# Performance work log

Hardware: AMD Instinct MI355X
Metric: run time of the kernel (lower is better)

The kernel has to match this reference:

```python
import jax, jax.numpy as jnp
import numpy as np
import math

# ---------- real Clebsch-Gordan coupling tables (computed once, tiny) ----------
def _cg(j1, m1, j2, m2, j3, m3):
    if m1 + m2 != m3 or j3 < abs(j1 - j2) or j3 > j1 + j2:
        return 0.0
    f = math.factorial
    pre = ((2 * j3 + 1) * f(j3 + j1 - j2) * f(j3 - j1 + j2) * f(j1 + j2 - j3) / f(j1 + j2 + j3 + 1)) ** 0.5
    pre *= (f(j3 + m3) * f(j3 - m3) * f(j1 - m1) * f(j1 + m1) * f(j2 - m2) * f(j2 + m2)) ** 0.5
    s = 0.0
    for k in range(0, j1 + j2 - j3 + 1):
        d = (k, j1 + j2 - j3 - k, j1 - m1 - k, j2 + m2 - k, j3 - j2 + m1 + k, j3 - j1 - m2 + k)
        if min(d) < 0:
            continue
        den = 1
        for t in d:
            den *= f(t)
        s += (-1) ** k / den
    return pre * s

def _Q(l):  # complex->real spherical-harmonic change of basis
    Q = np.zeros((2 * l + 1, 2 * l + 1), dtype=complex)
    Q[l, l] = 1.0
    s = 2 ** -0.5
    for m in range(1, l + 1):
        Q[l + m, l + m] = (-1) ** m * s
        Q[l + m, l - m] = s
        Q[l - m, l + m] = -1j * (-1) ** m * s
        Q[l - m, l - m] = 1j * s
    return Q

def _K(l1, l2, l3):  # real coupling tensor [2l3+1, 2l1+1, 2l2+1]
    C = np.zeros((2 * l3 + 1, 2 * l1 + 1, 2 * l2 + 1), dtype=complex)
    for M3 in range(-l3, l3 + 1):
        for M1 in range(-l1, l1 + 1):
            for M2 in range(-l2, l2 + 1):
                C[M3 + l3, M1 + l1, M2 + l2] = _cg(l1, M1, l2, M2, l3, M3)
    K = np.einsum('cC,aA,bB,CAB->cab', _Q(l3).conj(), _Q(l1), _Q(l2), C)
    K = K.imag if np.abs(K.imag).max() > np.abs(K.real).max() else K.real
    return np.asarray(K, dtype=np.float32)

# the 9 'uvu' instructions (in_l, edge_l, out_l) with multiplicities (weight_numel=144)
_PATHS = [(0, 0, 0), (0, 2, 2), (1, 0, 1), (1, 2, 1), (1, 2, 2), (2, 0, 2), (2, 2, 0), (2, 2, 1), (2, 2, 2)]
_KT = [jnp.asarray(_K(*p)) for p in _PATHS]
_MULS = [32, 32, 16, 16, 16, 8, 8, 8, 8]
_SPLITS = np.cumsum(_MULS)[:-1].tolist()
NEI = 8
EPS = 1e-5

def _sh(u):  # component-normalized real SH of unit vectors, l=0..2 (m order -l..l, l=1 -> y,z,x)
    x, y, z = u[:, 0], u[:, 1], u[:, 2]
    sh0 = jnp.ones_like(x)[:, None]
    sh1 = np.float32(3 ** 0.5) * jnp.stack([y, z, x], -1)
    s15 = np.float32(15 ** 0.5)
    s5 = np.float32(5 ** 0.5)
    sh2 = jnp.stack([s15 * x * y, s15 * y * z, 0.5 * s5 * (3 * z * z - 1.0), s15 * x * z, 0.5 * s15 * (x * x - y * y)], -1)
    return sh0, sh1, sh2

def _path(xs, sh, wp, Kt):  # xs [E,u,2l1+1], sh [E,2l2+1], Kt [2l3+1,2l1+1,2l2+1] -> [E,u,2l3+1]
    return jnp.einsum('eui,ej,oij->euo', xs, sh, Kt) * wp[None, :, None]

def _layer(x0, x1, x2, pos, src, dst, w, W0, W1, W2, bw0, bb0, bw1, bw2, N):
    ev = pos[dst] - pos[src]
    u = ev / (jnp.linalg.norm(ev, axis=1, keepdims=True) + 1e-12)
    sh0, sh1, sh2 = _sh(u)
    s0 = x0[src][:, :, None]  # [E,32,1]
    s1 = x1[src]              # [E,16,3]
    s2 = x2[src]              # [E,8,5]
    ws = jnp.split(w, _SPLITS)
    p1 = _path(s0, sh0, ws[0], _KT[0])
    p2 = _path(s0, sh2, ws[1], _KT[1])
    p3 = _path(s1, sh0, ws[2], _KT[2])
    p4 = _path(s1, sh2, ws[3], _KT[3])
    p5 = _path(s1, sh2, ws[4], _KT[4])
    p6 = _path(s2, sh0, ws[5], _KT[5])
    p7 = _path(s2, sh2, ws[6], _KT[6])
    p8 = _path(s2, sh2, ws[7], _KT[7])
    p9 = _path(s2, sh2, ws[8], _KT[8])
    m0 = jnp.concatenate([p1, p7], 1)          # [E,40,1]
    m1 = jnp.concatenate([p3, p4, p8], 1)      # [E,40,3]
    m2 = jnp.concatenate([p2, p5, p6, p9], 1)  # [E,64,5]
    a0 = jax.ops.segment_sum(m0, dst, num_segments=N)
    a1 = jax.ops.segment_sum(m1, dst, num_segments=N)
    a2 = jax.ops.segment_sum(m2, dst, num_segments=N)
    y0 = (a0[:, :, 0] @ W0) * np.float32(1.0 / 40 ** 0.5)
    y1 = jnp.einsum('num,uv->nvm', a1, W1) * np.float32(1.0 / 40 ** 0.5)
    y2 = jnp.einsum('num,uv->nvm', a2, W2) * np.float32(1.0 / 64 ** 0.5)
    # equivariant batchnorm (training stats): scalars -> standard BN, l>0 -> norm BN
    f = y0 - y0.mean(0)
    y0 = f / jnp.sqrt((f * f).mean(0) + EPS) * bw0 + bb0
    y1 = y1 / jnp.sqrt((y1 * y1).mean(axis=(0, 2)) + EPS)[None, :, None] * bw1[None, :, None]
    y2 = y2 / jnp.sqrt((y2 * y2).mean(axis=(0, 2)) + EPS)[None, :, None] * bw2[None, :, None]
    return y0, y1, y2

def _forward(positions, W_emb, tp_w, lin_W0, lin_W1, lin_W2, bn_w0, bn_b0, bn_w1, bn_w2, Wf1, Wf2, bf2, Wf3, bf3):
    B, P, _ = positions.shape
    N = B * P
    pos = positions.reshape(N, 3)
    # kNN graph from dense cdist + topk (indices are not differentiated)
    pg = jax.lax.stop_gradient(pos)
    sq = jnp.sum(pg * pg, 1)
    d2 = sq[:, None] + sq[None, :] - 2.0 * (pg @ pg.T)
    _, idx = jax.lax.top_k(-d2, NEI + 1)  # smallest distances; col 0 is self
    src = jnp.repeat(jnp.arange(N), NEI)
    dst = idx[:, 1:].reshape(-1)
    x0 = jnp.ones((N, 1), jnp.float32) @ W_emb  # embedding: only 0e->0e path exists
    x1 = jnp.zeros((N, 16, 3), jnp.float32)
    x2 = jnp.zeros((N, 8, 5), jnp.float32)
    for l in range(3):
        y0, y1, y2 = _layer(x0, x1, x2, pos, src, dst, tp_w[l], lin_W0[l], lin_W1[l], lin_W2[l],
                            bn_w0[l], bn_b0[l], bn_w1[l], bn_w2[l], N)
        x0 = jax.nn.relu(y0) + x0
        x1 = jax.nn.relu(y1) + x1
        x2 = jax.nn.relu(y2) + x2
    h = jax.nn.relu((x0 @ Wf1) * np.float32(1.0 / 32 ** 0.5))  # scalar part -> 32x0e
    h = jax.nn.relu(h @ Wf2 + bf2)
    out = (h @ Wf3 + bf3).reshape(B, P, 2)
    return out

def setup_inputs() -> dict:
    key = jax.random.key(0)
    ks = jax.random.split(key, 16)
    B, P = 4, 2048
    return {
        'positions': jax.random.normal(ks[0], (B, P, 3), jnp.float32) * 3.0,
        'W_emb': jax.random.normal(ks[1], (1, 32), jnp.float32),
        'tp_w': jax.random.normal(ks[2], (3, 144), jnp.float32),
        'lin_W0': jax.random.normal(ks[3], (3, 40, 32), jnp.float32),
        'lin_W1': jax.random.normal(ks[4], (3, 40, 16), jnp.float32),
        'lin_W2': jax.random.normal(ks[5], (3, 64, 8), jnp.float32),
        'bn_w0': 1.0 + 0.05 * jax.random.normal(ks[6], (3, 32), jnp.float32),
        'bn_b0': jnp.zeros((3, 32), jnp.float32),
        'bn_w1': 1.0 + 0.05 * jax.random.normal(ks[7], (3, 16), jnp.float32),
        'bn_w2': 1.0 + 0.05 * jax.random.normal(ks[8], (3, 8), jnp.float32),
        'Wf1': jax.random.normal(ks[9], (32, 32), jnp.float32),
        'Wf2': jax.random.normal(ks[10], (32, 16), jnp.float32) * 0.2,
        'bf2': jax.random.normal(ks[11], (16,), jnp.float32) * 0.1,
        'Wf3': jax.random.normal(ks[12], (16, 2), jnp.float32) * 0.2,
        'bf3': jax.random.normal(ks[13], (2,), jnp.float32) * 0.1,
    }

def reference(positions, W_emb, tp_w, lin_W0, lin_W1, lin_W2, bn_w0, bn_b0, bn_w1, bn_w2, Wf1, Wf2, bf2, Wf3, bf3):
    return _forward(positions, W_emb, tp_w, lin_W0, lin_W1, lin_W2, bn_w0, bn_b0, bn_w1, bn_w2, Wf1, Wf2, bf2, Wf3, bf3)
```

## Files before the change

### kernel.cpp

```cpp
#include <hip/hip_runtime.h>
#include <math.h>

#define NN 8192
#define REV_CAP 48
#define KNN_CAP 384
#define PF 12

static const size_t OFF_K     = 0;
static const size_t OFF_CNT   = 512;
static const size_t OFF_REV   = 8704;
static const size_t OFF_STATS = 401920;
static const size_t OFF_XF    = 406528;
static const size_t OFF_YF    = 1389568;
static const size_t WS_FLOATS = 2372608;

static double h_dfact(int n){ double r=1.0; for(int i=2;i<=n;++i) r*=(double)i; return r; }

static double h_dcg(int j1,int m1,int j2,int m2,int j3,int m3){
  if (m1+m2!=m3) return 0.0;
  if (j3 < abs(j1-j2) || j3 > j1+j2) return 0.0;
  double pre = sqrt((double)(2*j3+1)*h_dfact(j3+j1-j2)*h_dfact(j3-j1+j2)*h_dfact(j1+j2-j3)/h_dfact(j1+j2+j3+1));
  pre *= sqrt(h_dfact(j3+m3)*h_dfact(j3-m3)*h_dfact(j1-m1)*h_dfact(j1+m1)*h_dfact(j2-m2)*h_dfact(j2+m2));
  double s=0.0;
  for(int k=0;k<=j1+j2-j3;++k){
    int d1=j1+j2-j3-k, d2=j1-m1-k, d3=j2+m2-k, d4=j3-j2+m1+k, d5=j3-j1-m2+k;
    if(d1<0||d2<0||d3<0||d4<0||d5<0) continue;
    double den = h_dfact(k)*h_dfact(d1)*h_dfact(d2)*h_dfact(d3)*h_dfact(d4)*h_dfact(d5);
    s += ((k&1)? -1.0: 1.0)/den;
  }
  return pre*s;
}

static int h_qrow(int l,int r,int* col,double* re,double* im){
  const double s = 0.70710678118654752440;
  if (r==l){ col[0]=l; re[0]=1.0; im[0]=0.0; return 1; }
  if (r>l){ int m=r-l;
    col[0]=l+m; re[0]=((m&1)?-s:s); im[0]=0.0;
    col[1]=l-m; re[1]=s;            im[1]=0.0;
  } else { int m=l-r;
    col[0]=l+m; re[0]=0.0; im[0]=((m&1)? s : -s);
    col[1]=l-m; re[1]=0.0; im[1]=s;
  }
  return 2;
}

static float g_Khost[405];
static bool  g_Kinit = false;

static void h_computeK(){
  const int sizes[9]={1,25,9,45,75,25,25,75,125};
  const int l1s[9]={0,0,1,1,1,2,2,2,2};
  const int l2s[9]={0,2,0,2,2,0,2,2,2};
  const int l3s[9]={0,2,1,1,2,2,0,1,2};
  for(int tid=0; tid<405; ++tid){
    int p=0, rem=tid;
    for(p=0;p<9;++p){ if(rem < sizes[p]) break; rem -= sizes[p]; }
    const int l1=l1s[p], l2=l2s[p], l3=l3s[p];
    const int n1=2*l1+1, n2=2*l2+1;
    const int c = rem/(n1*n2); const int r2 = rem%(n1*n2); const int a=r2/n2; const int b=r2%n2;

    int c3[2],c1[2],c2[2]; double re3[2],im3[2],re1[2],im1[2],re2[2],im2[2];
    const int nc3 = h_qrow(l3,c,c3,re3,im3);
    const int nc1 = h_qrow(l1,a,c1,re1,im1);
    const int nc2 = h_qrow(l2,b,c2,re2,im2);

    double accRe=0, accIm=0;
    for(int i3=0;i3<nc3;++i3){
      const double q3re=re3[i3], q3im=-im3[i3];
      for(int i1=0;i1<nc1;++i1){
        const double pre_re = q3re*re1[i1] - q3im*im1[i1];
        const double pre_im = q3re*im1[i1] + q3im*re1[i1];
        for(int i2=0;i2<nc2;++i2){
          const double cgv = h_dcg(l1, c1[i1]-l1, l2, c2[i2]-l2, l3, c3[i3]-l3);
          if (cgv==0.0) continue;
          accRe += (pre_re*re2[i2] - pre_im*im2[i2])*cgv;
          accIm += (pre_re*im2[i2] + pre_im*re2[i2])*cgv;
        }
      }
    }
    const bool useImag = ((l1+l2+l3)&1)!=0;
    g_Khost[tid] = (float)(useImag? accIm : accRe);
  }
}

__global__ __launch_bounds__(256) void k_setup(const float* __restrict__ pos,
        const float* __restrict__ W_emb,
        float* __restrict__ xf,
        float* __restrict__ xs, float* __restrict__ ys, float* __restrict__ zs,
        float* __restrict__ qs,
        int* __restrict__ cnt, float* __restrict__ stats){
  int idx = blockIdx.x*256 + threadIdx.x;
  if (idx < 983040) { const int c = idx%120; xf[idx] = (c<32)? W_emb[c] : 0.f; return; }
  idx -= 983040;
  if (idx < 8192) {
    const float x=pos[3*idx], y=pos[3*idx+1], z=pos[3*idx+2];
    xs[idx]=x; ys[idx]=y; zs[idx]=z; qs[idx]=0.5f*(x*x+y*y+z*z);
    return;
  }
  idx -= 8192;
  if (idx < 8192) { cnt[idx]=0; return; }
  idx -= 8192;
  if (idx < 3072) stats[idx]=0.f;
}

__device__ __forceinline__ unsigned fkey(float f){
  const unsigned b = __float_as_uint(f);
  return (b & 0x80000000u) ? ~b : (b | 0x80000000u);
}

#define RSELECT_PUSH(KMAX) do{ \
  unsigned P = 0u; int need = 9; \
  _Pragma("unroll 1") \
  for(int bit=31; bit>=0; --bit){ \
    const unsigned pref = P >> bit; \
    int c0 = 0; \
    _Pragma("unroll") \
    for(int k=0;k<KMAX;++k) c0 += __popcll(__ballot((ku[k]>>bit)==pref)); \
    if (need > c0){ need -= c0; P |= (1u<<bit); } \
  } \
  int c_eq = 0; \
  _Pragma("unroll") \
  for(int k=0;k<KMAX;++k) c_eq += __popcll(__ballot(ku[k]==P)); \
  bool tsel[KMAX]; \
  _Pragma("unroll") \
  for(int k=0;k<KMAX;++k) tsel[k] = (ku[k]==P); \
  if (c_eq > need){ \
    _Pragma("unroll") \
    for(int k=0;k<KMAX;++k) tsel[k]=false; \
    for(int r=0;r<need;++r){ \
      int mid = 0x7fffffff; \
      _Pragma("unroll") \
      for(int k=0;k<KMAX;++k) if (ku[k]==P && !tsel[k] && il[k]<mid) mid = il[k]; \
      _Pragma("unroll") \
      for(int s=32;s>0;s>>=1){ const int om = __shfl_xor(mid,s,64); mid = (om<mid)? om : mid; } \
      _Pragma("unroll") \
      for(int k=0;k<KMAX;++k) if (ku[k]==P && il[k]==mid) tsel[k]=true; \
    } \
  } \
  _Pragma("unroll") \
  for(int k=0;k<KMAX;++k){ \
    const bool take = (ku[k] < P) || tsel[k]; \
    const int ix = il[k]; \
    if (take && ix != node){ \
      int cpos = atomicAdd(&cnt[ix],1); \
      if (cpos < REV_CAP) rev[ix*REV_CAP + cpos] = node; \
    } \
  } \
}while(0)

__global__ __launch_bounds__(256, 8) void k_knn8(const float* __restrict__ xs,
                                              const float* __restrict__ ys,
                                              const float* __restrict__ zs,
                                              const float* __restrict__ qs,
                                              int* __restrict__ cnt, int* __restrict__ rev){
  const int lane = threadIdx.x & 63;
  const int w    = threadIdx.x >> 6;
  const int node = blockIdx.x*4 + w;
  __shared__ float sdist[4][KNN_CAP];
  __shared__ int   sidx[4][KNN_CAP];
  __shared__ int   scount[4];
  if (threadIdx.x < 4) scount[threadIdx.x]=0;
  __syncthreads();

  const float px = xs[node], py = ys[node], pz = zs[node];

  float m1 = INFINITY, m2 = INFINITY;
  for(int c=0;c<4;++c){
    const int base = (c*64 + lane)*4;
    const float4 fx = *(const float4*)(xs + base);
    const float4 fy = *(const float4*)(ys + base);
    const float4 fz = *(const float4*)(zs + base);
    const float4 fq = *(const float4*)(qs + base);
    float ss[4];
    ss[0] = fmaf(-px,fx.x, fmaf(-py,fy.x, fmaf(-pz,fz.x, fq.x)));
    ss[1] = fmaf(-px,fx.y, fmaf(-py,fy.y, fmaf(-pz,fz.y, fq.y)));
    ss[2] = fmaf(-px,fx.z, fmaf(-py,fy.z, fmaf(-pz,fz.z, fq.z)));
    ss[3] = fmaf(-px,fx.w, fmaf(-py,fy.w, fmaf(-pz,fz.w, fq.w)));
    #pragma unroll
    for(int q=0;q<4;++q){
      const float hi = fmaxf(m1, ss[q]);
      m1 = fminf(m1, ss[q]);
      m2 = fminf(m2, hi);
    }
  }
  {
    const unsigned kk1 = fkey(m1), kk2 = fkey(m2);
    unsigned P = 0u; int need = 9;
    #pragma unroll 1
    for(int bit=31; bit>=0; --bit){
      const unsigned pref = P >> bit;
      const int c0 = __popcll(__ballot((kk1>>bit)==pref)) + __popcll(__ballot((kk2>>bit)==pref));
      if (need > c0){ need -= c0; P |= (1u<<bit); }
    }
    m1 = __uint_as_float((P & 0x80000000u) ? (P & 0x7fffffffu) : ~P);
  }
  const float T = m1;

  {
    const int b0 = lane*4;
    float4 nfx = *(const float4*)(xs + b0);
    float4 nfy = *(const float4*)(ys + b0);
    float4 nfz = *(const float4*)(zs + b0);
    float4 nfq = *(const float4*)(qs + b0);
    for(int c=0;c<32;++c){
      const float4 fx=nfx, fy=nfy, fz=nfz, fq=nfq;
      const int cbase = (c*64 + lane)*4;
      if (c<31){
        const int nb2 = ((c+1)*64 + lane)*4;
        nfx = *(const float4*)(xs + nb2);
        nfy = *(const float4*)(ys + nb2);
        nfz = *(const float4*)(zs + nb2);
        nfq = *(const float4*)(qs + nb2);
      }
      float ss[4];
      ss[0] = fmaf(-px,fx.x, fmaf(-py,fy.x, fmaf(-pz,fz.x, fq.x)));
      ss[1] = fmaf(-px,fx.y, fmaf(-py,fy.y, fmaf(-pz,fz.y, fq.y)));
      ss[2] = fmaf(-px,fx.z, fmaf(-py,fy.z, fmaf(-pz,fz.z, fq.z)));
      ss[3] = fmaf(-px,fx.w, fmaf(-py,fy.w, fmaf(-pz,fz.w, fq.w)));
      #pragma unroll
      for(int q=0;q<4;++q){
        if (ss[q] <= T){
          int pos = atomicAdd(&scount[w],1);
          if (pos < KNN_CAP){ sdist[w][pos]=ss[q]; sidx[w][pos]=cbase+q; }
        }
      }
    }
  }
  __syncthreads();

  int m = scount[w]; if (m > KNN_CAP) m = KNN_CAP;
  unsigned ku[KNN_CAP/64]; int il[KNN_CAP/64];
  #pragma unroll
  for(int k=0;k<KNN_CAP/64;++k){
    const int j = lane + 64*k;
    if (j < m){ ku[k]=fkey(sdist[w][j]); il[k]=sidx[w][j]; }
    else      { ku[k]=0xffffffffu;       il[k]=0x7fffffff; }
  }
  if (m <= 128) RSELECT_PUSH(2);
  else          RSELECT_PUSH(6);
}

__global__ __launch_bounds__(256) void k_msg(
  const float* __restrict__ pos,
  const int* __restrict__ cnt, const int* __restrict__ rev,
  const float* __restrict__ Kbuf,
  const float* __restrict__ xf,
  const float* __restrict__ tpw,
  const float* __restrict__ W0, const float* __restrict__ W1, const float* __restrict__ W2,
  float* __restrict__ pA, float* __restrict__ pB,
  float* __restrict__ yf)
{
  const int t = threadIdx.x;
  const int w = t >> 6;
  const int lane = t & 63;
  const int n = blockIdx.x*4 + w;

  __shared__ float KL[405];
  __shared__ float TW[144];
  __shared__ float momPS[4][720];
  __shared__ float aS[4][480];
  __shared__ int   eIdx[4][REV_CAP];
  __shared__ float eSh[4][5][REV_CAP];
  __shared__ float bA[32], bB[96];
  for(int q=t;q<405;q+=256) KL[q]=Kbuf[q];
  for(int q=t;q<144;q+=256) TW[q]=tpw[q];
  if (t<96){ bB[t]=0.f; if(t<32) bA[t]=0.f; }

  const int deg0 = cnt[n];
  const int deg = (deg0<REV_CAP)? deg0 : REV_CAP;
  const float pnx=pos[3*n], pny=pos[3*n+1], pnz=pos[3*n+2];
  const float s15 = 3.8729833462f, s5c = 2.2360679775f;
  if (lane < deg){
    const int i = rev[n*REV_CAP+lane];
    eIdx[w][lane] = i;
    const float ex = pnx - pos[3*i], ey = pny - pos[3*i+1], ez = pnz - pos[3*i+2];
    const float rn = sqrtf(ex*ex+ey*ey+ez*ez) + 1e-12f;
    const float ux=ex/rn, uy=ey/rn, uz=ez/rn;
    eSh[w][0][lane]=s15*ux*uy;
    eSh[w][1][lane]=s15*uy*uz;
    eSh[w][2][lane]=0.5f*s5c*(3.f*uz*uz-1.f);
    eSh[w][3][lane]=s15*ux*uz;
    eSh[w][4][lane]=0.5f*s15*(ux*ux-uy*uy);
  }
  __syncthreads();

  const int c0 = lane*2;
  float mp0=0.f, mp1=0.f;
  float ms0[5], ms1[5];
  #pragma unroll
  for(int j=0;j<5;++j){ ms0[j]=0.f; ms1[j]=0.f; }

  int idxr[PF];
  #pragma unroll
  for(int k=0;k<PF;++k) idxr[k] = (k<deg)? eIdx[w][k] : 0;
  float2 fr[PF];
  if (lane<60){
    #pragma unroll
    for(int k=0;k<PF;++k) fr[k] = *(const float2*)(xf + (size_t)idxr[k]*120 + c0);
  }
  #pragma unroll
  for(int k=0;k<PF;++k){
    if (k<deg){
      const float sh0=eSh[w][0][k], sh1=eSh[w][1][k], sh2=eSh[w][2][k];
      const float sh3=eSh[w][3][k], sh4=eSh[w][4][k];
      if (lane<60){
        const float2 f = fr[k];
        mp0 += f.x; mp1 += f.y;
        ms0[0]+=f.x*sh0; ms0[1]+=f.x*sh1; ms0[2]+=f.x*sh2; ms0[3]+=f.x*sh3; ms0[4]+=f.x*sh4;
        ms1[0]+=f.y*sh0; ms1[1]+=f.y*sh1; ms1[2]+=f.y*sh2; ms1[3]+=f.y*sh3; ms1[4]+=f.y*sh4;
      }
    }
  }
  for(int e=PF;e<deg;++e){
    const int i = eIdx[w][e];
    const float sh0=eSh[w][0][e], sh1=eSh[w][1][e], sh2=eSh[w][2][e];
    const float sh3=eSh[w][3][e], sh4=eSh[w][4][e];
    if (lane<60){
      const float2 f = *(const float2*)(xf + (size_t)i*120 + c0);
      mp0 += f.x; mp1 += f.y;
      ms0[0]+=f.x*sh0; ms0[1]+=f.x*sh1; ms0[2]+=f.x*sh2; ms0[3]+=f.x*sh3; ms0[4]+=f.x*sh4;
      ms1[0]+=f.y*sh0; ms1[1]+=f.y*sh1; ms1[2]+=f.y*sh2; ms1[3]+=f.y*sh3; ms1[4]+=f.y*sh4;
    }
  }
  if (lane<60){
    momPS[w][c0]=mp0; momPS[w][c0+1]=mp1;
    #pragma unroll
    for(int j=0;j<5;++j){ momPS[w][120+c0*5+j]=ms0[j]; momPS[w][120+(c0+1)*5+j]=ms1[j]; }
  }
  __syncthreads();

  #pragma unroll 1
  for(int e=lane; e<480; e+=64){
    int a, b, L, dst; float rw;
    if (e<32){        const int u=e;                            a=0;        b=u;                  L=1;  rw=TW[u];     dst=u; }
    else if (e<192){  const int i=e-32,  u=i/5, o=i%5;          a=1+o*5;    b=120+u*5;            L=5;  rw=TW[32+u];  dst=160+u*5+o; }
    else if (e<240){  const int i=e-192, u=i/3, o=i%3;          a=26+o*3;   b=32+u*3;             L=3;  rw=TW[64+u];  dst=40+u*3+o; }
    else if (e<288){  const int i=e-240, u=i/3, o=i%3;          a=35+o*15;  b=120+(32+u*3)*5;     L=15; rw=TW[80+u];  dst=40+(16+u)*3+o; }
    else if (e<368){  const int i=e-288, u=i/5, o=i%5;          a=80+o*15;  b=120+(32+u*3)*5;     L=15; rw=TW[96+u];  dst=160+(32+u)*5+o; }
    else if (e<408){  const int i=e-368, u=i/5, o=i%5;          a=155+o*5;  b=80+u*5;             L=5;  rw=TW[112+u]; dst=160+(48+u)*5+o; }
    else if (e<416){  const int u=e-408;                        a=180;      b=120+(80+u*5)*5;     L=25; rw=TW[120+u]; dst=32+u; }
    else if (e<440){  const int i=e-416, u=i/3, o=i%3;          a=205+o*25; b=120+(80+u*5)*5;     L=25; rw=TW[128+u]; dst=40+(32+u)*3+o; }
    else {            const int i=e-440, u=i/5, o=i%5;          a=280+o*25; b=120+(80+u*5)*5;     L=25; rw=TW[136+u]; dst=160+(56+u)*5+o; }
    float g=0.f;
    #pragma unroll 1
    for(int k=0;k<L;++k) g += KL[a+k]*momPS[w][b+k];
    aS[w][dst] = rw*g;
  }
  __syncthreads();

  const float inv40 = 0.15811388300841896660f;
  for(int q=lane;q<120;q+=64){
    float out; int chan;
    if (q<32){
      float g=0.f;
      for(int uu=0;uu<40;++uu) g += aS[w][uu]*W0[uu*32+q];
      out = g*inv40; chan = q;
    } else if (q<80){
      const int e=q-32, v=e/3, m=e%3;
      float g=0.f;
      for(int uu=0;uu<40;++uu) g += aS[w][40+uu*3+m]*W1[uu*16+v];
      out = g*inv40; chan = 32+v;
    } else {
      const int e=q-80, tt=e/5, m=e%5;
      float g=0.f;
      for(int uu=0;uu<64;++uu) g += aS[w][160+uu*5+m]*W2[uu*8+tt];
      out = g*0.125f; chan = 48+tt;
    }
    yf[(size_t)n*120+q] = out;
    atomicAdd(&bB[chan], out*out);
    if (q<32) atomicAdd(&bA[q], out);
  }
  __syncthreads();
  if (t<96){
    const int slot = blockIdx.x & 7;
    atomicAdd(&pB[slot*96 + t], bB[t]);
    if (t<32) atomicAdd(&pA[slot*32 + t], bA[t]);
  }
}

__global__ __launch_bounds__(256) void k_norm(const float* __restrict__ yf,
                       const float* __restrict__ pA, const float* __restrict__ pB,
                       const float* __restrict__ bw0,const float* __restrict__ bb0,
                       const float* __restrict__ bw1,const float* __restrict__ bw2,
                       float* __restrict__ xf){
  __shared__ float sc[96], sf[32];
  const int t = threadIdx.x;
  if (t<96){
    float sB=0.f;
    #pragma unroll
    for(int k=0;k<8;++k) sB += pB[k*96+t];
    float scale;
    if (t<32){
      float sA=0.f;
      #pragma unroll
      for(int k=0;k<8;++k) sA += pA[k*32+t];
      const float mean = sA*(1.f/8192.f);
      const float var  = sB*(1.f/8192.f) - mean*mean;
      const float inv  = 1.f/sqrtf(var+1e-5f);
      scale = bw0[t]*inv;
      sf[t] = bb0[t] - mean*scale;
    } else if (t<48){
      scale = bw1[t-32]/sqrtf(sB*(1.f/(8192.f*3.f))+1e-5f);
    } else {
      scale = bw2[t-48]/sqrtf(sB*(1.f/(8192.f*5.f))+1e-5f);
    }
    sc[t]=scale;
  }
  __syncthreads();
  const int idx = blockIdx.x*256 + t;
  if (idx >= NN*120) return;
  const int c = idx%120;
  const int chan = (c<32)? c : ((c<80)? 32+(c-32)/3 : 48+(c-80)/5);
  const float v = yf[idx]*sc[chan] + ((c<32)? sf[c] : 0.f);
  xf[idx] += fmaxf(v,0.f);
}

__global__ __launch_bounds__(256) void k_normmlp(const float* __restrict__ yf,
                                             const float* __restrict__ xf,
                                             const float* __restrict__ pA, const float* __restrict__ pB,
                                             const float* __restrict__ bw0,const float* __restrict__ bb0,
                                             const float* __restrict__ Wf1,const float* __restrict__ Wf2,
                                             const float* __restrict__ bf2,const float* __restrict__ Wf3,
                                             const float* __restrict__ bf3, float* __restrict__ out){
  __shared__ float w1[1024], w2[512], w3[32], b2[16], b3[2], sc0[32], sf0[32];
  const int t=threadIdx.x;
  for(int q=t;q<1024;q+=256) w1[q]=Wf1[q];
  for(int q=t;q<512;q+=256)  w2[q]=Wf2[q];
  if(t<32) w3[t]=Wf3[t];
  if(t<16) b2[t]=bf2[t];
  if(t<2)  b3[t]=bf3[t];
  if(t<32){
    float sA=0.f, sB=0.f;
    #pragma unroll
    for(int k=0;k<8;++k){ sA += pA[k*32+t]; sB += pB[k*96+t]; }
    const float mean = sA*(1.f/8192.f);
    const float var  = sB*(1.f/8192.f) - mean*mean;
    const float inv  = 1.f/sqrtf(var+1e-5f);
    sc0[t] = bw0[t]*inv;
    sf0[t] = bb0[t] - mean*sc0[t];
  }
  __syncthreads();
  const int n = blockIdx.x*256+t;
  if(n>=NN) return;
  float xv[32];
  #pragma unroll
  for(int k=0;k<32;++k){
    const float v = yf[(size_t)n*120+k]*sc0[k] + sf0[k];
    xv[k] = xf[(size_t)n*120+k] + fmaxf(v,0.f);
  }
  const float inv32 = 0.17677669529663688110f;
  float h1[32];
  #pragma unroll 4
  for(int c=0;c<32;++c){ float g=0.f;
    #pragma unroll
    for(int k=0;k<32;++k) g+=xv[k]*w1[k*32+c];
    h1[c]=fmaxf(g*inv32,0.f); }
  float h2[16];
  #pragma unroll 4
  for(int c=0;c<16;++c){ float g=b2[c];
    #pragma unroll
    for(int k=0;k<32;++k) g+=h1[k]*w2[k*16+c];
    h2[c]=fmaxf(g,0.f); }
  #pragma unroll
  for(int m=0;m<2;++m){ float g=b3[m];
    #pragma unroll
    for(int k=0;k<16;++k) g+=h2[k]*w3[k*2+m];
    out[n*2+m]=g; }
}

extern "C" void kernel_launch(void* const* d_in, const int* in_sizes, int n_in,
                              void* d_out, int out_size, void* d_ws, size_t ws_size,
                              hipStream_t stream) {
  const float* positions = (const float*)d_in[0];
  const float* W_emb  = (const float*)d_in[1];
  const float* tp_w   = (const float*)d_in[2];
  const float* lin_W0 = (const float*)d_in[3];
  const float* lin_W1 = (const float*)d_in[4];
  const float* lin_W2 = (const float*)d_in[5];
  const float* bn_w0  = (const float*)d_in[6];
  const float* bn_b0  = (const float*)d_in[7];
  const float* bn_w1  = (const float*)d_in[8];
  const float* bn_w2  = (const float*)d_in[9];
  const float* Wf1 = (const float*)d_in[10];
  const float* Wf2 = (const float*)d_in[11];
  const float* bf2 = (const float*)d_in[12];
  const float* Wf3 = (const float*)d_in[13];
  const float* bf3 = (const float*)d_in[14];

  if (ws_size < WS_FLOATS*sizeof(float)) return;

  float* ws    = (float*)d_ws;
  float* Kbuf  = ws + OFF_K;
  int*   cnt   = (int*)(ws + OFF_CNT);
  int*   rev   = (int*)(ws + OFF_REV);
  float* stats = ws + OFF_STATS;
  float* xf = ws + OFF_XF;
  float* yf = ws + OFF_YF;

  float* xs = yf;
  float* ysA = yf + NN;
  float* zs = yf + 2*NN;
  float* qs = yf + 3*NN;

  if (!g_Kinit){ h_computeK(); g_Kinit = true; }
  hipMemcpyAsync(Kbuf, g_Khost, 405*sizeof(float), hipMemcpyHostToDevice, stream);

  k_setup<<<3916,256,0,stream>>>(positions, W_emb, xf, xs, ysA, zs, qs, cnt, stats);
  k_knn8<<<NN/4,256,0,stream>>>(xs, ysA, zs, qs, cnt, rev);

  for(int l=0;l<3;++l){
    float* pA = stats + l*1024;
    float* pB = pA + 256;
    k_msg<<<NN/4,256,0,stream>>>(positions, cnt, rev, Kbuf, xf,
                              tp_w + l*144, lin_W0 + l*40*32, lin_W1 + l*40*16, lin_W2 + l*64*8,
                              pA, pB, yf);
    if (l<2){
      k_norm<<<(NN*120+255)/256,256,0,stream>>>(yf, pA, pB,
                              bn_w0 + l*32, bn_b0 + l*32, bn_w1 + l*16, bn_w2 + l*8,
                              xf);
    }
  }
  k_normmlp<<<NN/256,256,0,stream>>>(yf, xf, stats + 2*1024, stats + 2*1024 + 256,
                              bn_w0 + 64, bn_b0 + 64,
                              Wf1, Wf2, bf2, Wf3, bf3, (float*)d_out);
}
```

Measured before the change: 277.3 us.

## Process two query nodes per wavefront in kNN and parallelize final MLP per node

The kNN kernel now has each wavefront handle two query nodes, so every candidate position load serves two distance computations. This halves global/L2 traffic per node at the cost of more registers and twice the shared candidate buffers per block. The final norm+MLP kernel switches from one thread per node with large register arrays to one wavefront per node, with lanes computing output channels through shared memory. That raises parallelism for the 8192-node tail kernel but adds block-wide syncs and leaves most lanes idle.

```diff
diff --git a/kernel.cpp b/kernel.cpp
--- a/kernel.cpp
+++ b/kernel.cpp
@@ -106,6 +106,18 @@
 __device__ __forceinline__ unsigned fkey(float f){
   const unsigned b = __float_as_uint(f);
   return (b & 0x80000000u) ? ~b : (b | 0x80000000u);
+}
+
+__device__ __forceinline__ float rsel9_T(float m1, float m2){
+  const unsigned kk1 = fkey(m1), kk2 = fkey(m2);
+  unsigned P = 0u; int need = 9;
+  #pragma unroll 1
+  for(int bit=31; bit>=0; --bit){
+    const unsigned pref = P >> bit;
+    const int c0 = __popcll(__ballot((kk1>>bit)==pref)) + __popcll(__ballot((kk2>>bit)==pref));
+    if (need > c0){ need -= c0; P |= (1u<<bit); }
+  }
+  return __uint_as_float((P & 0x80000000u) ? (P & 0x7fffffffu) : ~P);
 }
 
 #define RSELECT_PUSH(KMAX) do{ \
@@ -155,46 +167,39 @@
                                               int* __restrict__ cnt, int* __restrict__ rev){
   const int lane = threadIdx.x & 63;
   const int w    = threadIdx.x >> 6;
-  const int node = blockIdx.x*4 + w;
-  __shared__ float sdist[4][KNN_CAP];
-  __shared__ int   sidx[4][KNN_CAP];
-  __shared__ int   scount[4];
-  if (threadIdx.x < 4) scount[threadIdx.x]=0;
-  __syncthreads();
-
-  const float px = xs[node], py = ys[node], pz = zs[node];
-
-  float m1 = INFINITY, m2 = INFINITY;
+  const int n0   = blockIdx.x*8 + w*2;
+  const int w2   = w*2;
+  __shared__ float sdist[8][KNN_CAP];
+  __shared__ int   sidx[8][KNN_CAP];
+  __shared__ int   scount[8];
+  if (threadIdx.x < 8) scount[threadIdx.x]=0;
+  __syncthreads();
+
+  const float px0 = xs[n0],   py0 = ys[n0],   pz0 = zs[n0];
+  const float px1 = xs[n0+1], py1 = ys[n0+1], pz1 = zs[n0+1];
+
+  float m1a=INFINITY, m2a=INFINITY, m1b=INFINITY, m2b=INFINITY;
   for(int c=0;c<4;++c){
     const int base = (c*64 + lane)*4;
     const float4 fx = *(const float4*)(xs + base);
     const float4 fy = *(const float4*)(ys + base);
     const float4 fz = *(const float4*)(zs + base);
     const float4 fq = *(const float4*)(qs + base);
-    float ss[4];
-    ss[0] = fmaf(-px,fx.x, fmaf(-py,fy.x, fmaf(-pz,fz.x, fq.x)));
-    ss[1] = fmaf(-px,fx.y, fmaf(-py,fy.y, fmaf(-pz,fz.y, fq.y)));
-    ss[2] = fmaf(-px,fx.z, fmaf(-py,fy.z, fmaf(-pz,fz.z, fq.z)));
-    ss[3] = fmaf(-px,fx.w, fmaf(-py,fy.w, fmaf(-pz,fz.w, fq.w)));
+    const float cx[4]={fx.x,fx.y,fx.z,fx.w};
+    const float cy[4]={fy.x,fy.y,fy.z,fy.w};
+    const float cz[4]={fz.x,fz.y,fz.z,fz.w};
+    const float cq[4]={fq.x,fq.y,fq.z,fq.w};
     #pragma unroll
     for(int q=0;q<4;++q){
-      const float hi = fmaxf(m1, ss[q]);
-      m1 = fminf(m1, ss[q]);
-      m2 = fminf(m2, hi);
-    }
-  }
-  {
-    const unsigned kk1 = fkey(m1), kk2 = fkey(m2);
-    unsigned P = 0u; int need = 9;
-    #pragma unroll 1
-    for(int bit=31; bit>=0; --bit){
-      const unsigned pref = P >> bit;
-      const int c0 = __popcll(__ballot((kk1>>bit)==pref)) + __popcll(__ballot((kk2>>bit)==pref));
-      if (need > c0){ need -= c0; P |= (1u<<bit); }
-    }
-    m1 = __uint_as_float((P & 0x80000000u) ? (P & 0x7fffffffu) : ~P);
-  }
-  const float T = m1;
+      const float s0 = fmaf(-px0,cx[q], fmaf(-py0,cy[q], fmaf(-pz0,cz[q], cq[q])));
+      const float s1 = fmaf(-px1,cx[q], fmaf(-py1,cy[q], fmaf(-pz1,cz[q], cq[q])));
+      float hi;
+      hi = fmaxf(m1a, s0); m1a = fminf(m1a, s0); m2a = fminf(m2a, hi);
+      hi = fmaxf(m1b, s1); m1b = fminf(m1b, s1); m2b = fminf(m2b, hi);
+    }
+  }
+  const float T0 = rsel9_T(m1a, m2a);
+  const float T1 = rsel9_T(m1b, m2b);
 
   {
     const int b0 = lane*4;
@@ -212,32 +217,42 @@
         nfz = *(const float4*)(zs + nb2);
         nfq = *(const float4*)(qs + nb2);
       }
-      float ss[4];
-      ss[0] = fmaf(-px,fx.x, fmaf(-py,fy.x, fmaf(-pz,fz.x, fq.x)));
-      ss[1] = fmaf(-px,fx.y, fmaf(-py,fy.y, fmaf(-pz,fz.y, fq.y)));
-      ss[2] = fmaf(-px,fx.z, fmaf(-py,fy.z, fmaf(-pz,fz.z, fq.z)));
-      ss[3] = fmaf(-px,fx.w, fmaf(-py,fy.w, fmaf(-pz,fz.w, fq.w)));
+      const float cx[4]={fx.x,fx.y,fx.z,fx.w};
+      const float cy[4]={fy.x,fy.y,fy.z,fy.w};
+      const float cz[4]={fz.x,fz.y,fz.z,fz.w};
+      const float cq[4]={fq.x,fq.y,fq.z,fq.w};
       #pragma unroll
       for(int q=0;q<4;++q){
-        if (ss[q] <= T){
-          int pos = atomicAdd(&scount[w],1);
-          if (pos < KNN_CAP){ sdist[w][pos]=ss[q]; sidx[w][pos]=cbase+q; }
+        const float s0 = fmaf(-px0,cx[q], fmaf(-py0,cy[q], fmaf(-pz0,cz[q], cq[q])));
+        const float s1 = fmaf(-px1,cx[q], fmaf(-py1,cy[q], fmaf(-pz1,cz[q], cq[q])));
+        if (s0 <= T0){
+          int pos = atomicAdd(&scount[w2],1);
+          if (pos < KNN_CAP){ sdist[w2][pos]=s0; sidx[w2][pos]=cbase+q; }
+        }
+        if (s1 <= T1){
+          int pos = atomicAdd(&scount[w2+1],1);
+          if (pos < KNN_CAP){ sdist[w2+1][pos]=s1; sidx[w2+1][pos]=cbase+q; }
         }
       }
     }
   }
   __syncthreads();
 
-  int m = scount[w]; if (m > KNN_CAP) m = KNN_CAP;
-  unsigned ku[KNN_CAP/64]; int il[KNN_CAP/64];
-  #pragma unroll
-  for(int k=0;k<KNN_CAP/64;++k){
-    const int j = lane + 64*k;
-    if (j < m){ ku[k]=fkey(sdist[w][j]); il[k]=sidx[w][j]; }
-    else      { ku[k]=0xffffffffu;       il[k]=0x7fffffff; }
-  }
-  if (m <= 128) RSELECT_PUSH(2);
-  else          RSELECT_PUSH(6);
+  #pragma unroll 1
+  for(int u=0;u<2;++u){
+    const int node = n0+u;
+    const int s_   = w2+u;
+    int m = scount[s_]; if (m > KNN_CAP) m = KNN_CAP;
+    unsigned ku[KNN_CAP/64]; int il[KNN_CAP/64];
+    #pragma unroll
+    for(int k=0;k<KNN_CAP/64;++k){
+      const int j = lane + 64*k;
+      if (j < m){ ku[k]=fkey(sdist[s_][j]); il[k]=sidx[s_][j]; }
+      else      { ku[k]=0xffffffffu;        il[k]=0x7fffffff; }
+    }
+    if (m <= 128) RSELECT_PUSH(2);
+    else          RSELECT_PUSH(6);
+  }
 }
 
 __global__ __launch_bounds__(256) void k_msg(
@@ -423,7 +438,10 @@
                                              const float* __restrict__ bf2,const float* __restrict__ Wf3,
                                              const float* __restrict__ bf3, float* __restrict__ out){
   __shared__ float w1[1024], w2[512], w3[32], b2[16], b3[2], sc0[32], sf0[32];
+  __shared__ float xvS[4][32], h1S[4][32], h2S[4][16];
   const int t=threadIdx.x;
+  const int w = t>>6, lane = t&63;
+  const int n = blockIdx.x*4 + w;
   for(int q=t;q<1024;q+=256) w1[q]=Wf1[q];
   for(int q=t;q<512;q+=256)  w2[q]=Wf2[q];
   if(t<32) w3[t]=Wf3[t];
@@ -440,32 +458,32 @@
     sf0[t] = bb0[t] - mean*sc0[t];
   }
   __syncthreads();
-  const int n = blockIdx.x*256+t;
-  if(n>=NN) return;
-  float xv[32];
-  #pragma unroll
-  for(int k=0;k<32;++k){
-    const float v = yf[(size_t)n*120+k]*sc0[k] + sf0[k];
-    xv[k] = xf[(size_t)n*120+k] + fmaxf(v,0.f);
-  }
+  if (lane<32){
+    const float v = yf[(size_t)n*120+lane]*sc0[lane] + sf0[lane];
+    xvS[w][lane] = xf[(size_t)n*120+lane] + fmaxf(v,0.f);
+  }
+  __syncthreads();
   const float inv32 = 0.17677669529663688110f;
-  float h1[32];
-  #pragma unroll 4
-  for(int c=0;c<32;++c){ float g=0.f;
-    #pragma unroll
-    for(int k=0;k<32;++k) g+=xv[k]*w1[k*32+c];
-    h1[c]=fmaxf(g*inv32,0.f); }
-  float h2[16];
-  #pragma unroll 4
-  for(int c=0;c<16;++c){ float g=b2[c];
-    #pragma unroll
-    for(int k=0;k<32;++k) g+=h1[k]*w2[k*16+c];
-    h2[c]=fmaxf(g,0.f); }
-  #pragma unroll
-  for(int m=0;m<2;++m){ float g=b3[m];
-    #pragma unroll
-    for(int k=0;k<16;++k) g+=h2[k]*w3[k*2+m];
-    out[n*2+m]=g; }
+  if (lane<32){
+    float g=0.f;
+    #pragma unroll 8
+    for(int k=0;k<32;++k) g += xvS[w][k]*w1[k*32+lane];
+    h1S[w][lane] = fmaxf(g*inv32, 0.f);
+  }
+  __syncthreads();
+  if (lane<16){
+    float g=b2[lane];
+    #pragma unroll 8
+    for(int k=0;k<32;++k) g += h1S[w][k]*w2[k*16+lane];
+    h2S[w][lane]=fmaxf(g,0.f);
+  }
+  __syncthreads();
+  if (lane<2){
+    float g=b3[lane];
+    #pragma unroll
+    for(int k=0;k<16;++k) g += h2S[w][k]*w3[k*2+lane];
+    out[n*2+lane]=g;
+  }
 }
 
 extern "C" void kernel_launch(void* const* d_in, const int* in_sizes, int n_in,
@@ -506,7 +524,7 @@
   hipMemcpyAsync(Kbuf, g_Khost, 405*sizeof(float), hipMemcpyHostToDevice, stream);
 
   k_setup<<<3916,256,0,stream>>>(positions, W_emb, xf, xs, ysA, zs, qs, cnt, stats);
-  k_knn8<<<NN/4,256,0,stream>>>(xs, ysA, zs, qs, cnt, rev);
+  k_knn8<<<NN/8,256,0,stream>>>(xs, ysA, zs, qs, cnt, rev);
 
   for(int l=0;l<3;++l){
     float* pA = stats + l*1024;
@@ -520,7 +538,7 @@
                               xf);
     }
   }
-  k_normmlp<<<NN/256,256,0,stream>>>(yf, xf, stats + 2*1024, stats + 2*1024 + 256,
+  k_normmlp<<<NN/4,256,0,stream>>>(yf, xf, stats + 2*1024, stats + 2*1024 + 256,
                               bn_w0 + 64, bn_b0 + 64,
                               Wf1, Wf2, bf2, Wf3, bf3, (float*)d_out);
 }
```

New measurement: 268.5 us (median of 2 runs). -3.2%, faster.
